# Kernel tuning notes

Hardware: AMD Instinct MI355X
Metric: run time of the kernel (lower is better)

Reference implementation:

```python
import jax, jax.numpy as jnp
import numpy as np

EPS_KERNEL = 1e-4   # eps added inside softmax_kernel exp
EPS_DENOM = 1e-6    # eps added to k_cumsum in the denominator
N_CHUNKS = 128      # matches torch.chunk(128, dim=-2) in causal_linear_attention_noncuda


def gaussian_orthogonal_random_matrix(nb_rows, nb_cols, rng):
    # scaling=0: rows are orthogonal blocks scaled by chi-distributed norms
    n_full = nb_rows // nb_cols + (1 if nb_rows % nb_cols else 0)
    blocks = []
    for _ in range(n_full):
        g = rng.standard_normal((nb_cols, nb_cols))
        qmat, _ = np.linalg.qr(g)
        blocks.append(qmat.T)
    mat = np.concatenate(blocks, axis=0)[:nb_rows]
    multiplier = np.linalg.norm(rng.standard_normal((nb_rows, nb_cols)), axis=1)
    return (multiplier[:, None] * mat).astype(np.float32)


def softmax_kernel(x, proj, is_query):
    # x: [b,h,n,d], proj: [m,d] -> phi(x): [b,h,n,m]
    d = x.shape[-1]
    normalizer = d ** -0.25
    ratio = proj.shape[0] ** -0.5
    xd = jnp.einsum('bhnd,md->bhnm', normalizer * x, proj)
    diag = 0.5 * (normalizer ** 2) * jnp.sum(x * x, axis=-1, keepdims=True)  # [b,h,n,1]
    if is_query:
        mx = jnp.max(xd, axis=-1, keepdims=True)
    else:
        mx = jnp.max(xd, axis=(-1, -2), keepdims=True)
    return ratio * (jnp.exp(xd - diag - mx) + EPS_KERNEL)


def causal_linear_attention(q, k, v):
    # q,k: [b,h,n,m] phi-features; v: [b,h,n,d]
    b, h, n, m = q.shape
    d = v.shape[-1]
    c = n // N_CHUNKS  # chunk length

    def chunked(t):
        return jnp.moveaxis(t.reshape(b, h, N_CHUNKS, c, t.shape[-1]), 2, 0)

    qc, kc, vc = chunked(q), chunked(k), chunked(v)  # [nc,b,h,c,*]

    def step(carry, inp):
        k_last, ctx_last = carry  # [b,h,m], [b,h,m,d]
        qi, ki, vi = inp
        k_cum = k_last[:, :, None, :] + jnp.cumsum(ki, axis=2)            # [b,h,c,m]
        d_inv = 1.0 / jnp.einsum('bhcm,bhcm->bhc', qi, k_cum + EPS_DENOM)
        ctx = jnp.einsum('bhcm,bhcd->bhcmd', ki, vi)                      # [b,h,c,m,d]
        ctx_cum = ctx_last[:, :, None, :, :] + jnp.cumsum(ctx, axis=2)
        out = jnp.einsum('bhcmd,bhcm,bhc->bhcd', ctx_cum, qi, d_inv)
        return (k_cum[:, :, -1], ctx_cum[:, :, -1]), out

    init = (jnp.zeros((b, h, m), q.dtype), jnp.zeros((b, h, m, d), q.dtype))
    _, outs = jax.lax.scan(jax.checkpoint(step), init, (qc, kc, vc))
    return jnp.moveaxis(outs, 0, 2).reshape(b, h, n, d)


def setup_inputs() -> dict:
    key = jax.random.key(0)
    kq, kk, kv = jax.random.split(key, 3)
    shape = (2, 8, 2048, 64)  # [batch, heads, seq, dim_heads]
    q = jax.random.normal(kq, shape, dtype=jnp.float32)
    k = jax.random.normal(kk, shape, dtype=jnp.float32)
    v = jax.random.normal(kv, shape, dtype=jnp.float32)
    proj = jnp.asarray(gaussian_orthogonal_random_matrix(256, 64, np.random.default_rng(0)))
    return {"q": q, "k": k, "v": v, "projection_matrix": proj}


def reference(q, k, v, projection_matrix):
    q_prime = softmax_kernel(q, projection_matrix, is_query=True)
    k_prime = softmax_kernel(k, projection_matrix, is_query=False)
    return causal_linear_attention(q_prime, k_prime, v)
```

## Files before the change

### kernel.cpp

```cpp
#include <hip/hip_runtime.h>
#include <hip/hip_bf16.h>
#include <cstddef>

typedef __attribute__((ext_vector_type(8))) short bf16x8;
typedef __attribute__((ext_vector_type(4))) float f32x4;

#define NCH_ 512
#define NRM_ 0.35355339059327373f
#define RATIO_ 0.0625f
#define EPSC_ 6.25e-6f
#define MFMA(a,b,c) __builtin_amdgcn_mfma_f32_16x16x32_bf16((a),(b),(c),0,0,0)

__device__ __forceinline__ unsigned short f2b(float f) {
  unsigned u = __float_as_uint(f);
  u += 0x7FFFu + ((u >> 16) & 1u);
  return (unsigned short)(u >> 16);
}
__device__ __forceinline__ float b2f(unsigned short h) {
  return __uint_as_float(((unsigned)h) << 16);
}
__device__ __forceinline__ unsigned pk2f(float a, float b) {
  union { __hip_bfloat162 h; unsigned u; } cv;
  cv.h = __float22bfloat162_rn(make_float2(a, b));
  return cv.u;
}
__device__ __forceinline__ float sumsq4(float4 a){ return a.x*a.x+a.y*a.y+a.z*a.z+a.w*a.w; }

__device__ __forceinline__ void gbar(unsigned* cnt, unsigned goal) {
  __syncthreads();
  if (threadIdx.x == 0) {
    __threadfence();
    __hip_atomic_fetch_add(cnt, 1u, __ATOMIC_RELEASE, __HIP_MEMORY_SCOPE_AGENT);
    while (__hip_atomic_fetch_add(cnt, 0u, __ATOMIC_RELAXED, __HIP_MEMORY_SCOPE_AGENT) < goal)
      __builtin_amdgcn_s_sleep(2);
    __threadfence();
  }
  __syncthreads();
}

__global__ __launch_bounds__(256, 2) void fused_kernel(
    const float* __restrict__ qg, const float* __restrict__ kg,
    const float* __restrict__ vg, const float* __restrict__ projg,
    unsigned short* __restrict__ kvxP, unsigned short* __restrict__ sxP,
    float* __restrict__ blockmax, float* __restrict__ vsumG,
    float* __restrict__ out_g, unsigned* __restrict__ barcnt)
{
  __shared__ unsigned short R0[256*72];
  __shared__ unsigned short XB[128*72];
  __shared__ unsigned short C_[80*72];
  __shared__ float diagK[64];
  __shared__ float diagQ[64];
  __shared__ float rmS[4*64];
  __shared__ float cmS[4];
  __shared__ float schS;
  const int t=threadIdx.x, ch=blockIdx.x;
  const int row0 = ch*64;
  const int lane=t&63, m16=lane&15, q4=lane>>4, w=t>>6;
  const int f0 = w*64, r0 = w*16;
  unsigned short* KX = XB;
  unsigned short* QX = XB + 64*72;
  unsigned short* kpT = XB;

#pragma unroll
  for (int i=0;i<8;++i){ int flat=i*2048+t*8; int f=flat>>6, d2=flat&63;
    float4 p0 = *(const float4*)(projg+flat);
    float4 p1 = *(const float4*)(projg+flat+4);
    *(uint4*)&R0[f*72+d2] = make_uint4(pk2f(p0.x,p0.y),pk2f(p0.z,p0.w),
                                       pk2f(p1.x,p1.y),pk2f(p1.z,p1.w)); }
  {
    const float* xg = kg + (size_t)row0*64;
#pragma unroll
    for (int i=0;i<4;++i){
      int flat=i*1024+t*4; int r=flat>>6, d2=flat&63;
      float4 f = *(const float4*)(xg+flat);
      float ss = sumsq4(f);
      ss += __shfl_xor(ss,1); ss += __shfl_xor(ss,2);
      ss += __shfl_xor(ss,4); ss += __shfl_xor(ss,8);
      if ((t&15)==0) diagK[r] = 0.0625f*ss;
      *(uint2*)&KX[r*72+d2] = make_uint2(pk2f(NRM_*f.x,NRM_*f.y), pk2f(NRM_*f.z,NRM_*f.w));
    }
  }
  {
    const float* xg = qg + (size_t)row0*64;
#pragma unroll
    for (int i=0;i<4;++i){
      int flat=i*1024+t*4; int r=flat>>6, d2=flat&63;
      float4 f = *(const float4*)(xg+flat);
      float ss = sumsq4(f);
      ss += __shfl_xor(ss,1); ss += __shfl_xor(ss,2);
      ss += __shfl_xor(ss,4); ss += __shfl_xor(ss,8);
      if ((t&15)==0) diagQ[r] = 0.0625f*ss;
      *(uint2*)&QX[r*72+d2] = make_uint2(pk2f(NRM_*f.x,NRM_*f.y), pk2f(NRM_*f.z,NRM_*f.w));
    }
  }
  {
    int c = t&63, sq_ = t>>6;
#pragma unroll
    for (int i=0;i<16;++i)
      C_[c*72 + sq_*16 + i] = f2b(vg[((size_t)row0 + sq_*16 + i)*64 + c]);
    int cc = 64 + (t>>4), s4 = (t&15)*4;
    unsigned short hv = (cc==64) ? (unsigned short)0x3F80 : (unsigned short)0;
    unsigned pv = (unsigned)hv | ((unsigned)hv<<16);
    *(uint2*)&C_[cc*72 + s4] = make_uint2(pv, pv);
  }
  __syncthreads();

  if (t < 80) {
    float s = 0.f;
#pragma unroll 16
    for (int i=0;i<64;++i) s += b2f(C_[t*72+i]);
    vsumG[(size_t)ch*80 + t] = s;
  }

  bf16x8 bk[4][2], bq[4][2]; float dk4[4], dq4[4];
#pragma unroll
  for (int rt=0;rt<4;++rt){
    bk[rt][0] = *(const bf16x8*)&KX[(rt*16+m16)*72 + q4*8];
    bk[rt][1] = *(const bf16x8*)&KX[(rt*16+m16)*72 + 32 + q4*8];
    bq[rt][0] = *(const bf16x8*)&QX[(rt*16+m16)*72 + q4*8];
    bq[rt][1] = *(const bf16x8*)&QX[(rt*16+m16)*72 + 32 + q4*8];
    dk4[rt] = diagK[rt*16+m16];
    dq4[rt] = diagQ[rt*16+m16];
  }
  f32x4 kacc[4][4], qacc[4][4];
#pragma unroll
  for (int rt=0;rt<4;++rt)
#pragma unroll
    for (int mt=0;mt<4;++mt){ kacc[rt][mt] = (f32x4){0.f,0.f,0.f,0.f};
                              qacc[rt][mt] = (f32x4){0.f,0.f,0.f,0.f}; }
#pragma unroll
  for (int kk=0;kk<2;++kk)
#pragma unroll
    for (int mt=0;mt<4;++mt){
      bf16x8 a = *(const bf16x8*)&R0[(f0+mt*16+m16)*72 + kk*32 + q4*8];
#pragma unroll
      for (int rt=0;rt<4;++rt){
        kacc[rt][mt] = MFMA(a, bk[rt][kk], kacc[rt][mt]);
        qacc[rt][mt] = MFMA(a, bq[rt][kk], qacc[rt][mt]);
      }
    }
  {
    float mx = kacc[0][0][0];
#pragma unroll
    for (int rt=0;rt<4;++rt)
#pragma unroll
      for (int mt=0;mt<4;++mt)
#pragma unroll
        for (int j=0;j<4;++j) mx = fmaxf(mx, kacc[rt][mt][j]);
#pragma unroll
    for (int off=1; off<64; off<<=1) mx = fmaxf(mx, __shfl_xor(mx, off));
    if (lane == 0) cmS[w] = mx;
  }
#pragma unroll
  for (int rt=0;rt<4;++rt){
    float p = qacc[rt][0][0];
#pragma unroll
    for (int mt=0;mt<4;++mt)
#pragma unroll
      for (int j=0;j<4;++j) p = fmaxf(p, qacc[rt][mt][j]);
    p = fmaxf(p, __shfl_xor(p,16)); p = fmaxf(p, __shfl_xor(p,32));
    if (q4 == 0) rmS[w*64 + rt*16+m16] = p;
  }
  __syncthreads();
  const float cmax = fmaxf(fmaxf(cmS[0],cmS[1]),fmaxf(cmS[2],cmS[3]));
  if (t == 0) blockmax[ch] = cmax;

  unsigned short* qS = R0;
#pragma unroll
  for (int rt=0;rt<4;++rt){
    int rr = rt*16+m16;
    float rm = fmaxf(fmaxf(rmS[rr],rmS[64+rr]),fmaxf(rmS[128+rr],rmS[192+rr]));
    float e = dq4[rt] + rm;
#pragma unroll
    for (int mt=0;mt<4;++mt){
      float v0 = RATIO_*(__expf(qacc[rt][mt][0]-e)+1e-4f);
      float v1 = RATIO_*(__expf(qacc[rt][mt][1]-e)+1e-4f);
      float v2 = RATIO_*(__expf(qacc[rt][mt][2]-e)+1e-4f);
      float v3 = RATIO_*(__expf(qacc[rt][mt][3]-e)+1e-4f);
      *(uint2*)&qS[rr*264 + f0 + mt*16 + q4*4] = make_uint2(pk2f(v0,v1), pk2f(v2,v3));
    }
  }
  __syncthreads();
  bf16x8 aq[8];
#pragma unroll
  for (int kk=0;kk<8;++kk)
    aq[kk] = *(const bf16x8*)&qS[(r0+m16)*264 + kk*32 + q4*8];
  float q1v = 0.f;
#pragma unroll
  for (int kk=0;kk<8;++kk){
    union { bf16x8 v; unsigned u[4]; } av; av.v = aq[kk];
#pragma unroll
    for (int i=0;i<4;++i)
      q1v += b2f((unsigned short)av.u[i]) + b2f((unsigned short)(av.u[i]>>16));
  }
  q1v += __shfl_xor(q1v,16); q1v += __shfl_xor(q1v,32);
  __syncthreads();

  unsigned short* kpS = R0;
  unsigned kpx[4][4][2];
#pragma unroll
  for (int rt=0;rt<4;++rt){
    float e = dk4[rt] + cmax;
    int rr = rt*16+m16;
#pragma unroll
    for (int mt=0;mt<4;++mt){
      float v0 = RATIO_*__expf(kacc[rt][mt][0]-e);
      float v1 = RATIO_*__expf(kacc[rt][mt][1]-e);
      float v2 = RATIO_*__expf(kacc[rt][mt][2]-e);
      float v3 = RATIO_*__expf(kacc[rt][mt][3]-e);
      kpx[rt][mt][0] = pk2f(v0,v1); kpx[rt][mt][1] = pk2f(v2,v3);
      *(uint2*)&kpS[rr*264 + f0 + mt*16 + q4*4] = make_uint2(kpx[rt][mt][0], kpx[rt][mt][1]);
    }
  }
  if ((w>>1) == 0) {
#pragma unroll
    for (int rt=0;rt<4;++rt)
#pragma unroll
      for (int mt=0;mt<4;++mt)
#pragma unroll
        for (int jp=0;jp<2;++jp){
          int frl = (w&1)*64 + mt*16 + q4*4 + jp*2;
          unsigned uv = kpx[rt][mt][jp];
          kpT[frl*72 + rt*16+m16]     = (unsigned short)uv;
          kpT[(frl+1)*72 + rt*16+m16] = (unsigned short)(uv>>16);
        }
  }
  __syncthreads();
#pragma unroll
  for (int h=0; h<2; ++h) {
    if (h == 1) {
      __syncthreads();
      if ((w>>1) == 1) {
#pragma unroll
        for (int rt=0;rt<4;++rt)
#pragma unroll
          for (int mt=0;mt<4;++mt)
#pragma unroll
            for (int jp=0;jp<2;++jp){
              int frl = (w&1)*64 + mt*16 + q4*4 + jp*2;
              unsigned uv = kpx[rt][mt][jp];
              kpT[frl*72 + rt*16+m16]     = (unsigned short)uv;
              kpT[(frl+1)*72 + rt*16+m16] = (unsigned short)(uv>>16);
            }
      }
      __syncthreads();
    }
    f32x4 c2a[5][2];
#pragma unroll
    for (int ct=0;ct<5;++ct)
#pragma unroll
      for (int p=0;p<2;++p) c2a[ct][p] = (f32x4){0.f,0.f,0.f,0.f};
#pragma unroll
    for (int kk=0;kk<2;++kk){
      bf16x8 av[5];
#pragma unroll
      for (int ct=0;ct<5;++ct)
        av[ct] = *(const bf16x8*)&C_[(ct*16+m16)*72 + kk*32 + q4*8];
#pragma unroll
      for (int p=0;p<2;++p){
        int mtl = w*2 + p;
        bf16x8 bv = *(const bf16x8*)&kpT[(mtl*16+m16)*72 + kk*32 + q4*8];
#pragma unroll
        for (int ct=0;ct<5;++ct)
          c2a[ct][p] = MFMA(av[ct], bv, c2a[ct][p]);
      }
    }
#pragma unroll
    for (int ct=0;ct<5;++ct)
#pragma unroll
      for (int p=0;p<2;++p){
        int mtg = h*8 + w*2 + p;
        int mrow = mtg*16 + m16;
        int fb = (mrow>>5)*512 + ((mrow>>3)&3)*8 + (mrow&7);
        unsigned short* dst = kvxP + (size_t)(ch*5+ct)*4096 + fb + (q4*4)*32;
#pragma unroll
        for (int j=0;j<4;++j)
          dst[j*32] = f2b(c2a[ct][p][j]);
      }
    if (h == 0) __syncthreads();
  }

  gbar(barcnt, (unsigned)gridDim.x);

  if (t < 32) {
    float bm = blockmax[(ch>>5)*32 + t];
    float km = bm;
#pragma unroll
    for (int off=16; off>=1; off>>=1) km = fmaxf(km, __shfl_xor(km, off));
    if (t == (ch & 31)) schS = __expf(bm - km);
  }
  if (ch < 320) {
    float* sS  = (float*)XB;
    float* vsS = ((float*)XB) + 32;
    const int qtr = ch & 3, ct5 = (ch>>2)%5, bh = ch/20;
    if (t < 32) {
      float bm = blockmax[bh*32 + t];
      float km = bm;
#pragma unroll
      for (int off=16; off>=1; off>>=1) km = fmaxf(km, __shfl_xor(km, off));
      sS[t] = __expf(bm - km);
    }
    for (int i=t; i<512; i+=256){
      int chl = i>>4, c16 = i&15;
      vsS[chl*16+c16] = vsumG[(size_t)(bh*32+chl)*80 + ct5*16 + c16];
    }
    __syncthreads();
    const int fbase = qtr*1024 + t*4;
    const int c16t = (t>>3)&15;
    const bool isEps = (ct5==4) && (c16t == 1);
    float carry0=0.f, carry1=0.f, carry2=0.f, carry3=0.f;
    const size_t stride = (size_t)5*4096;
    size_t base = ((size_t)(bh*32)*5 + ct5)*4096 + fbase;
#pragma unroll 4
    for (int chl=0; chl<32; ++chl){
      unsigned s0, s1;
      if (isEps) { unsigned ee = pk2f(1e-6f,1e-6f); s0 = ee; s1 = ee; }
      else { s0 = pk2f(carry0,carry1); s1 = pk2f(carry2,carry3); }
      *(uint2*)(sxP + base) = make_uint2(s0, s1);
      uint2 raw = *(const uint2*)(kvxP + base);
      float sc_ = sS[chl];
      float evs = EPSC_ * vsS[chl*16+c16t];
      carry0 += sc_*b2f((unsigned short)(raw.x))     + evs;
      carry1 += sc_*b2f((unsigned short)(raw.x>>16)) + evs;
      carry2 += sc_*b2f((unsigned short)(raw.y))     + evs;
      carry3 += sc_*b2f((unsigned short)(raw.y>>16)) + evs;
      base += stride;
    }
  }

  gbar(barcnt, 2u*(unsigned)gridDim.x);

  f32x4 accA[4], accO[5];
#pragma unroll
  for (int i=0;i<4;++i) accA[i] = (f32x4){0.f,0.f,0.f,0.f};
#pragma unroll
  for (int i=0;i<5;++i) accO[i] = (f32x4){0.f,0.f,0.f,0.f};
  const unsigned short* sxb = sxP + (size_t)ch*5*4096 + m16*32 + q4*8;
#pragma unroll
  for (int kk=0;kk<8;++kk){
    bf16x8 a = aq[kk];
#pragma unroll
    for (int st=0;st<4;++st){
      bf16x8 bfr = *(const bf16x8*)&kpS[(st*16+m16)*264 + kk*32 + q4*8];
      accA[st] = MFMA(a, bfr, accA[st]);
    }
#pragma unroll
    for (int ct=0;ct<5;++ct)
      accO[ct] = MFMA(a, *(const bf16x8*)(sxb + (size_t)ct*4096 + kk*512), accO[ct]);
  }
  __syncthreads();
  const float sch = schS;
  unsigned short* P = XB;
#pragma unroll
  for (int j=0;j<4;++j){
    int rr = r0 + q4*4 + j;
    float q1r = __shfl(q1v, q4*4 + j);
    float addc = EPSC_ * q1r;
#pragma unroll
    for (int st=0;st<4;++st){
      int cc = st*16 + m16;
      P[rr*72 + cc] = f2b((cc<=rr) ? (sch*accA[st][j] + addc) : 0.f);
    }
  }
#pragma unroll
  for (int k2=0;k2<2;++k2){
    bf16x8 aP = *(const bf16x8*)&P[(r0+m16)*72 + k2*32 + q4*8];
#pragma unroll
    for (int ct=0;ct<5;++ct){
      bf16x8 bfr = *(const bf16x8*)&C_[(ct*16+m16)*72 + k2*32 + q4*8];
      accO[ct] = MFMA(aP, bfr, accO[ct]);
    }
  }
  __syncthreads();
  float* oT = (float*)R0;
#pragma unroll
  for (int j=0;j<4;++j){
    float d64 = __shfl(accO[4][j], (lane & 48));
    float d65 = __shfl(accO[4][j], (lane & 48) | 1);
    float dinv = 1.f/(d64+d65);
    int rr = r0 + q4*4 + j;
#pragma unroll
    for (int ct=0;ct<4;++ct)
      oT[rr*68 + ct*16 + m16] = accO[ct][j]*dinv;
  }
  __syncthreads();
#pragma unroll
  for (int i=0;i<4;++i){ int flat=i*1024+t*4; int r=flat>>6, c2=flat&63;
    *(float4*)(out_g + (size_t)row0*64 + flat) = *(const float4*)&oT[r*68+c2]; }
}


__global__ __launch_bounds__(256, 2) void kfeat_kernel(
    const float* __restrict__ kg, const float* __restrict__ vg,
    const float* __restrict__ projg,
    unsigned short* __restrict__ kvxP,
    float* __restrict__ blockmax, float* __restrict__ vsumG)
{
  __shared__ unsigned short R0[256*72];
  __shared__ unsigned short XB[128*72];
  __shared__ unsigned short C_[80*72];
  __shared__ float diagS[64];
  __shared__ float rmS[4];
  const int t=threadIdx.x, ch=blockIdx.x;
  const int row0 = ch*64;
  const int lane=t&63, m16=lane&15, q4=lane>>4, w=t>>6;
  const int f0 = w*64;
  unsigned short* kpS = R0;
  unsigned short* xbS = XB;
  unsigned short* kpT = XB;

#pragma unroll
  for (int i=0;i<8;++i){ int flat=i*2048+t*8; int f=flat>>6, d2=flat&63;
    float4 p0 = *(const float4*)(projg+flat);
    float4 p1 = *(const float4*)(projg+flat+4);
    *(uint4*)&R0[f*72+d2] = make_uint4(pk2f(p0.x,p0.y),pk2f(p0.z,p0.w),
                                       pk2f(p1.x,p1.y),pk2f(p1.z,p1.w)); }
  {
    const float* xg = kg + (size_t)row0*64;
#pragma unroll
    for (int i=0;i<4;++i){
      int flat=i*1024+t*4; int r=flat>>6, d2=flat&63;
      float4 f = *(const float4*)(xg+flat);
      float ss = sumsq4(f);
      ss += __shfl_xor(ss,1); ss += __shfl_xor(ss,2);
      ss += __shfl_xor(ss,4); ss += __shfl_xor(ss,8);
      if ((t&15)==0) diagS[r] = 0.0625f*ss;
      *(uint2*)&xbS[r*72+d2] = make_uint2(pk2f(NRM_*f.x,NRM_*f.y), pk2f(NRM_*f.z,NRM_*f.w));
    }
  }
  {
    int c = t&63, sq_ = t>>6;
#pragma unroll
    for (int i=0;i<16;++i)
      C_[c*72 + sq_*16 + i] = f2b(vg[((size_t)row0 + sq_*16 + i)*64 + c]);
    int cc = 64 + (t>>4), s4 = (t&15)*4;
    unsigned short hv = (cc==64) ? (unsigned short)0x3F80 : (unsigned short)0;
    unsigned pv = (unsigned)hv | ((unsigned)hv<<16);
    *(uint2*)&C_[cc*72 + s4] = make_uint2(pv, pv);
  }
  __syncthreads();

  if (t < 80) {
    float s = 0.f;
#pragma unroll 16
    for (int i=0;i<64;++i) s += b2f(C_[t*72+i]);
    vsumG[(size_t)ch*80 + t] = s;
  }

  bf16x8 b[4][2]; float diag4[4];
#pragma unroll
  for (int rt=0;rt<4;++rt){
    b[rt][0] = *(const bf16x8*)&xbS[(rt*16+m16)*72 + q4*8];
    b[rt][1] = *(const bf16x8*)&xbS[(rt*16+m16)*72 + 32 + q4*8];
    diag4[rt] = diagS[rt*16+m16];
  }
  f32x4 acc[4][4];
#pragma unroll
  for (int rt=0;rt<4;++rt)
#pragma unroll
    for (int mt=0;mt<4;++mt) acc[rt][mt] = (f32x4){0.f,0.f,0.f,0.f};
#pragma unroll
  for (int kk=0;kk<2;++kk)
#pragma unroll
    for (int mt=0;mt<4;++mt){
      bf16x8 a = *(const bf16x8*)&R0[(f0+mt*16+m16)*72 + kk*32 + q4*8];
#pragma unroll
      for (int rt=0;rt<4;++rt)
        acc[rt][mt] = MFMA(a, b[rt][kk], acc[rt][mt]);
    }
  {
    float mx = acc[0][0][0];
#pragma unroll
    for (int rt=0;rt<4;++rt)
#pragma unroll
      for (int mt=0;mt<4;++mt)
#pragma unroll
        for (int j=0;j<4;++j) mx = fmaxf(mx, acc[rt][mt][j]);
#pragma unroll
    for (int off=1; off<64; off<<=1) mx = fmaxf(mx, __shfl_xor(mx, off));
    if (lane == 0) rmS[w] = mx;
  }
  __syncthreads();
  const float cmax = fmaxf(fmaxf(rmS[0],rmS[1]),fmaxf(rmS[2],rmS[3]));
  if (t == 0) blockmax[ch] = cmax;

  unsigned kpx[4][4][2];
#pragma unroll
  for (int rt=0;rt<4;++rt){
    float e = diag4[rt] + cmax;
    int rr = rt*16+m16;
#pragma unroll
    for (int mt=0;mt<4;++mt){
      float v0 = RATIO_*__expf(acc[rt][mt][0]-e);
      float v1 = RATIO_*__expf(acc[rt][mt][1]-e);
      float v2 = RATIO_*__expf(acc[rt][mt][2]-e);
      float v3 = RATIO_*__expf(acc[rt][mt][3]-e);
      kpx[rt][mt][0] = pk2f(v0,v1); kpx[rt][mt][1] = pk2f(v2,v3);
      *(uint2*)&kpS[rr*264 + f0 + mt*16 + q4*4] = make_uint2(kpx[rt][mt][0], kpx[rt][mt][1]);
    }
  }
  if ((w>>1) == 0) {
#pragma unroll
    for (int rt=0;rt<4;++rt)
#pragma unroll
      for (int mt=0;mt<4;++mt)
#pragma unroll
        for (int jp=0;jp<2;++jp){
          int frl = (w&1)*64 + mt*16 + q4*4 + jp*2;
          unsigned uv = kpx[rt][mt][jp];
          kpT[frl*72 + rt*16+m16]     = (unsigned short)uv;
          kpT[(frl+1)*72 + rt*16+m16] = (unsigned short)(uv>>16);
        }
  }
  __syncthreads();
#pragma unroll
  for (int h=0; h<2; ++h) {
    if (h == 1) {
      __syncthreads();
      if ((w>>1) == 1) {
#pragma unroll
        for (int rt=0;rt<4;++rt)
#pragma unroll
          for (int mt=0;mt<4;++mt)
#pragma unroll
            for (int jp=0;jp<2;++jp){
              int frl = (w&1)*64 + mt*16 + q4*4 + jp*2;
              unsigned uv = kpx[rt][mt][jp];
              kpT[frl*72 + rt*16+m16]     = (unsigned short)uv;
              kpT[(frl+1)*72 + rt*16+m16] = (unsigned short)(uv>>16);
            }
      }
      __syncthreads();
    }
    f32x4 c2a[5][2];
#pragma unroll
    for (int ct=0;ct<5;++ct)
#pragma unroll
      for (int p=0;p<2;++p) c2a[ct][p] = (f32x4){0.f,0.f,0.f,0.f};
#pragma unroll
    for (int kk=0;kk<2;++kk){
      bf16x8 av[5];
#pragma unroll
      for (int ct=0;ct<5;++ct)
        av[ct] = *(const bf16x8*)&C_[(ct*16+m16)*72 + kk*32 + q4*8];
#pragma unroll
      for (int p=0;p<2;++p){
        int mtl = w*2 + p;
        bf16x8 bv = *(const bf16x8*)&kpT[(mtl*16+m16)*72 + kk*32 + q4*8];
#pragma unroll
        for (int ct=0;ct<5;++ct)
          c2a[ct][p] = MFMA(av[ct], bv, c2a[ct][p]);
      }
    }
#pragma unroll
    for (int ct=0;ct<5;++ct)
#pragma unroll
      for (int p=0;p<2;++p){
        int mtg = h*8 + w*2 + p;
        int mrow = mtg*16 + m16;
        int fb = (mrow>>5)*512 + ((mrow>>3)&3)*8 + (mrow&7);
        unsigned short* dst = kvxP + (size_t)(ch*5+ct)*4096 + fb + (q4*4)*32;
#pragma unroll
        for (int j=0;j<4;++j)
          dst[j*32] = f2b(c2a[ct][p][j]);
      }
    if (h == 0) __syncthreads();
  }
}

__global__ __launch_bounds__(256, 4) void scan_kernel(
    const unsigned short* __restrict__ kvxP, unsigned short* __restrict__ sxP,
    const float* __restrict__ blockmax, const float* __restrict__ vsumG)
{
  __shared__ float sS[32];
  __shared__ float vsS[32][16];
  const int t = threadIdx.x, bid = blockIdx.x;
  const int qtr = bid & 3, ct = (bid>>2)%5, bh = bid/20;
  if (t < 32) {
    float bm = blockmax[bh*32 + t];
    float km = bm;
#pragma unroll
    for (int off=16; off>=1; off>>=1) km = fmaxf(km, __shfl_xor(km, off));
    sS[t] = __expf(bm - km);
  }
  for (int i=t; i<512; i+=256){
    int chl = i>>4, c16 = i&15;
    vsS[chl][c16] = vsumG[(size_t)(bh*32+chl)*80 + ct*16 + c16];
  }
  __syncthreads();
  const int fbase = qtr*1024 + t*4;
  const int c16t = (t>>3)&15;
  const bool isEps = (ct==4) && (c16t == 1);
  float carry0=0.f, carry1=0.f, carry2=0.f, carry3=0.f;
  const size_t stride = (size_t)5*4096;
  size_t base = ((size_t)(bh*32)*5 + ct)*4096 + fbase;
#pragma unroll 4
  for (int chl=0; chl<32; ++chl){
    unsigned s0, s1;
    if (isEps) { unsigned ee = pk2f(1e-6f,1e-6f); s0 = ee; s1 = ee; }
    else { s0 = pk2f(carry0,carry1); s1 = pk2f(carry2,carry3); }
    *(uint2*)(sxP + base) = make_uint2(s0, s1);
    uint2 raw = *(const uint2*)(kvxP + base);
    float sch = sS[chl];
    float evs = EPSC_ * vsS[chl][c16t];
    carry0 += sch*b2f((unsigned short)(raw.x))     + evs;
    carry1 += sch*b2f((unsigned short)(raw.x>>16)) + evs;
    carry2 += sch*b2f((unsigned short)(raw.y))     + evs;
    carry3 += sch*b2f((unsigned short)(raw.y>>16)) + evs;
    base += stride;
  }
}

__global__ __launch_bounds__(256, 2) void out_kernel(
    const float* __restrict__ qg, const float* __restrict__ kg,
    const float* __restrict__ projg, const unsigned short* __restrict__ sxP,
    const float* __restrict__ vg, const float* __restrict__ blockmax,
    float* __restrict__ out_g)
{
  __shared__ unsigned short R0[256*72];
  __shared__ unsigned short KX[64*72];
  __shared__ unsigned short QX[64*72];
  __shared__ unsigned short C_[80*72];
  __shared__ float diagK[64];
  __shared__ float diagQ[64];
  __shared__ float rmS[4*64];
  __shared__ float cmS[4];
  __shared__ float schS;
  const int t=threadIdx.x, ch=blockIdx.x;
  const int row0 = ch*64;
  const int lane=t&63, m16=lane&15, q4=lane>>4, w=t>>6;
  const int f0 = w*64, r0 = w*16;
  unsigned short* P = KX;

#pragma unroll
  for (int i=0;i<8;++i){ int flat=i*2048+t*8; int f=flat>>6, d2=flat&63;
    float4 p0 = *(const float4*)(projg+flat);
    float4 p1 = *(const float4*)(projg+flat+4);
    *(uint4*)&R0[f*72+d2] = make_uint4(pk2f(p0.x,p0.y),pk2f(p0.z,p0.w),
                                       pk2f(p1.x,p1.y),pk2f(p1.z,p1.w)); }
  {
    const float* xg = kg + (size_t)row0*64;
#pragma unroll
    for (int i=0;i<4;++i){
      int flat=i*1024+t*4; int r=flat>>6, d2=flat&63;
      float4 f = *(const float4*)(xg+flat);
      float ss = sumsq4(f);
      ss += __shfl_xor(ss,1); ss += __shfl_xor(ss,2);
      ss += __shfl_xor(ss,4); ss += __shfl_xor(ss,8);
      if ((t&15)==0) diagK[r] = 0.0625f*ss;
      *(uint2*)&KX[r*72+d2] = make_uint2(pk2f(NRM_*f.x,NRM_*f.y), pk2f(NRM_*f.z,NRM_*f.w));
    }
  }
  {
    const float* xg = qg + (size_t)row0*64;
#pragma unroll
    for (int i=0;i<4;++i){
      int flat=i*1024+t*4; int r=flat>>6, d2=flat&63;
      float4 f = *(const float4*)(xg+flat);
      float ss = sumsq4(f);
      ss += __shfl_xor(ss,1); ss += __shfl_xor(ss,2);
      ss += __shfl_xor(ss,4); ss += __shfl_xor(ss,8);
      if ((t&15)==0) diagQ[r] = 0.0625f*ss;
      *(uint2*)&QX[r*72+d2] = make_uint2(pk2f(NRM_*f.x,NRM_*f.y), pk2f(NRM_*f.z,NRM_*f.w));
    }
  }
  {
    int c = t&63, sq_ = t>>6;
#pragma unroll
    for (int i=0;i<16;++i)
      C_[c*72 + sq_*16 + i] = f2b(vg[((size_t)row0 + sq_*16 + i)*64 + c]);
    int cc = 64 + (t>>4), s4 = (t&15)*4;
    unsigned short hv = (cc==64) ? (unsigned short)0x3F80 : (unsigned short)0;
    unsigned pv = (unsigned)hv | ((unsigned)hv<<16);
    *(uint2*)&C_[cc*72 + s4] = make_uint2(pv, pv);
  }
  if (t < 32) {
    float bm = blockmax[(ch>>5)*32 + t];
    float km = bm;
#pragma unroll
    for (int off=16; off>=1; off>>=1) km = fmaxf(km, __shfl_xor(km, off));
    if (t == (ch & 31)) schS = __expf(bm - km);
  }
  __syncthreads();

  bf16x8 bk[4][2], bq[4][2]; float dk4[4], dq4[4];
#pragma unroll
  for (int rt=0;rt<4;++rt){
    bk[rt][0] = *(const bf16x8*)&KX[(rt*16+m16)*72 + q4*8];
    bk[rt][1] = *(const bf16x8*)&KX[(rt*16+m16)*72 + 32 + q4*8];
    bq[rt][0] = *(const bf16x8*)&QX[(rt*16+m16)*72 + q4*8];
    bq[rt][1] = *(const bf16x8*)&QX[(rt*16+m16)*72 + 32 + q4*8];
    dk4[rt] = diagK[rt*16+m16];
    dq4[rt] = diagQ[rt*16+m16];
  }
  f32x4 kacc[4][4], qacc[4][4];
#pragma unroll
  for (int rt=0;rt<4;++rt)
#pragma unroll
    for (int mt=0;mt<4;++mt){ kacc[rt][mt] = (f32x4){0.f,0.f,0.f,0.f};
                              qacc[rt][mt] = (f32x4){0.f,0.f,0.f,0.f}; }
#pragma unroll
  for (int kk=0;kk<2;++kk)
#pragma unroll
    for (int mt=0;mt<4;++mt){
      bf16x8 a = *(const bf16x8*)&R0[(f0+mt*16+m16)*72 + kk*32 + q4*8];
#pragma unroll
      for (int rt=0;rt<4;++rt){
        kacc[rt][mt] = MFMA(a, bk[rt][kk], kacc[rt][mt]);
        qacc[rt][mt] = MFMA(a, bq[rt][kk], qacc[rt][mt]);
      }
    }
  {
    float mx = kacc[0][0][0];
#pragma unroll
    for (int rt=0;rt<4;++rt)
#pragma unroll
      for (int mt=0;mt<4;++mt)
#pragma unroll
        for (int j=0;j<4;++j) mx = fmaxf(mx, kacc[rt][mt][j]);
#pragma unroll
    for (int off=1; off<64; off<<=1) mx = fmaxf(mx, __shfl_xor(mx, off));
    if (lane == 0) cmS[w] = mx;
  }
#pragma unroll
  for (int rt=0;rt<4;++rt){
    float p = qacc[rt][0][0];
#pragma unroll
    for (int mt=0;mt<4;++mt)
#pragma unroll
      for (int j=0;j<4;++j) p = fmaxf(p, qacc[rt][mt][j]);
    p = fmaxf(p, __shfl_xor(p,16)); p = fmaxf(p, __shfl_xor(p,32));
    if (q4 == 0) rmS[w*64 + rt*16+m16] = p;
  }
  __syncthreads();
  const float cmax = fmaxf(fmaxf(cmS[0],cmS[1]),fmaxf(cmS[2],cmS[3]));

  unsigned short* qS = R0;
#pragma unroll
  for (int rt=0;rt<4;++rt){
    int rr = rt*16+m16;
    float rm = fmaxf(fmaxf(rmS[rr],rmS[64+rr]),fmaxf(rmS[128+rr],rmS[192+rr]));
    float e = dq4[rt] + rm;
#pragma unroll
    for (int mt=0;mt<4;++mt){
      float v0 = RATIO_*(__expf(qacc[rt][mt][0]-e)+1e-4f);
      float v1 = RATIO_*(__expf(qacc[rt][mt][1]-e)+1e-4f);
      float v2 = RATIO_*(__expf(qacc[rt][mt][2]-e)+1e-4f);
      float v3 = RATIO_*(__expf(qacc[rt][mt][3]-e)+1e-4f);
      *(uint2*)&qS[rr*264 + f0 + mt*16 + q4*4] = make_uint2(pk2f(v0,v1), pk2f(v2,v3));
    }
  }
  __syncthreads();
  bf16x8 aq[8];
#pragma unroll
  for (int kk=0;kk<8;++kk)
    aq[kk] = *(const bf16x8*)&qS[(r0+m16)*264 + kk*32 + q4*8];
  float q1v = 0.f;
#pragma unroll
  for (int kk=0;kk<8;++kk){
    union { bf16x8 v; unsigned u[4]; } av; av.v = aq[kk];
#pragma unroll
    for (int i=0;i<4;++i)
      q1v += b2f((unsigned short)av.u[i]) + b2f((unsigned short)(av.u[i]>>16));
  }
  q1v += __shfl_xor(q1v,16); q1v += __shfl_xor(q1v,32);
  __syncthreads();

  unsigned short* kpS = R0;
#pragma unroll
  for (int rt=0;rt<4;++rt){
    float e = dk4[rt] + cmax;
    int rr = rt*16+m16;
#pragma unroll
    for (int mt=0;mt<4;++mt){
      float v0 = RATIO_*__expf(kacc[rt][mt][0]-e);
      float v1 = RATIO_*__expf(kacc[rt][mt][1]-e);
      float v2 = RATIO_*__expf(kacc[rt][mt][2]-e);
      float v3 = RATIO_*__expf(kacc[rt][mt][3]-e);
      *(uint2*)&kpS[rr*264 + f0 + mt*16 + q4*4] = make_uint2(pk2f(v0,v1), pk2f(v2,v3));
    }
  }
  __syncthreads();

  f32x4 accA[4], accO[5];
#pragma unroll
  for (int i=0;i<4;++i) accA[i] = (f32x4){0.f,0.f,0.f,0.f};
#pragma unroll
  for (int i=0;i<5;++i) accO[i] = (f32x4){0.f,0.f,0.f,0.f};
  const unsigned short* sxb = sxP + (size_t)ch*5*4096 + m16*32 + q4*8;
#pragma unroll
  for (int kk=0;kk<8;++kk){
    bf16x8 a = aq[kk];
#pragma unroll
    for (int st=0;st<4;++st){
      bf16x8 bfr = *(const bf16x8*)&kpS[(st*16+m16)*264 + kk*32 + q4*8];
      accA[st] = MFMA(a, bfr, accA[st]);
    }
#pragma unroll
    for (int ct=0;ct<5;++ct)
      accO[ct] = MFMA(a, *(const bf16x8*)(sxb + (size_t)ct*4096 + kk*512), accO[ct]);
  }
  __syncthreads();
  const float sch = schS;
#pragma unroll
  for (int j=0;j<4;++j){
    int rr = r0 + q4*4 + j;
    float q1r = __shfl(q1v, q4*4 + j);
    float addc = EPSC_ * q1r;
#pragma unroll
    for (int st=0;st<4;++st){
      int cc = st*16 + m16;
      P[rr*72 + cc] = f2b((cc<=rr) ? (sch*accA[st][j] + addc) : 0.f);
    }
  }
#pragma unroll
  for (int k2=0;k2<2;++k2){
    bf16x8 aP = *(const bf16x8*)&P[(r0+m16)*72 + k2*32 + q4*8];
#pragma unroll
    for (int ct=0;ct<5;++ct){
      bf16x8 bfr = *(const bf16x8*)&C_[(ct*16+m16)*72 + k2*32 + q4*8];
      accO[ct] = MFMA(aP, bfr, accO[ct]);
    }
  }
  __syncthreads();
  float* oT = (float*)R0;
#pragma unroll
  for (int j=0;j<4;++j){
    float d64 = __shfl(accO[4][j], (lane & 48));
    float d65 = __shfl(accO[4][j], (lane & 48) | 1);
    float dinv = 1.f/(d64+d65);
    int rr = r0 + q4*4 + j;
#pragma unroll
    for (int ct=0;ct<4;++ct)
      oT[rr*68 + ct*16 + m16] = accO[ct][j]*dinv;
  }
  __syncthreads();
#pragma unroll
  for (int i=0;i<4;++i){ int flat=i*1024+t*4; int r=flat>>6, c2=flat&63;
    *(float4*)(out_g + (size_t)row0*64 + flat) = *(const float4*)&oT[r*68+c2]; }
}

extern "C" void kernel_launch(void* const* d_in, const int* in_sizes, int n_in,
                              void* d_out, int out_size, void* d_ws, size_t ws_size,
                              hipStream_t stream)
{
  (void)in_sizes; (void)n_in; (void)out_size; (void)ws_size;
  const float* q    = (const float*)d_in[0];
  const float* k    = (const float*)d_in[1];
  const float* v    = (const float*)d_in[2];
  const float* proj = (const float*)d_in[3];
  float* out = (float*)d_out;

  char* p8 = (char*)d_ws;
  unsigned short* kvxP = (unsigned short*)p8; p8 += (size_t)NCH_*5*4096*2;
  unsigned short* sxP  = (unsigned short*)p8; p8 += (size_t)NCH_*5*4096*2;
  float* blockmax = (float*)p8; p8 += NCH_*sizeof(float);
  float* vsumG    = (float*)p8; p8 += (size_t)NCH_*80*sizeof(float);
  unsigned* barcnt = (unsigned*)p8;

  static int fused_ok = -1;
  if (fused_ok < 0) {
    int nb = 0;
    hipError_t e = hipOccupancyMaxActiveBlocksPerMultiprocessor(&nb, fused_kernel,
                                                                256, (size_t)0);
    fused_ok = (e == hipSuccess && nb >= 2) ? 1 : 0;
  }

  if (fused_ok) {
    hipMemsetAsync(barcnt, 0, sizeof(unsigned), stream);
    fused_kernel<<<dim3(NCH_), dim3(256), 0, stream>>>(q, k, v, proj, kvxP, sxP,
                                                       blockmax, vsumG, out, barcnt);
  } else {
    kfeat_kernel<<<dim3(NCH_), dim3(256), 0, stream>>>(k, v, proj, kvxP,
                                                       blockmax, vsumG);
    scan_kernel <<<dim3(320),  dim3(256), 0, stream>>>(kvxP, sxP, blockmax, vsumG);
    out_kernel  <<<dim3(NCH_), dim3(256), 0, stream>>>(q, k, proj, sxP, v,
                                                       blockmax, out);
  }
}
```

Baseline: 115.2 us.

## Replace grid-wide barriers with per-(batch,head) arrival counters in fused kernel

The two global grid barriers become per-(batch,head) counters. Scan blocks wait only for the 32 feature blocks of their own head, and output blocks wait only for the 20 scan blocks that cover their head. This lets heads proceed independently and removes whole-grid stalls, at the cost of 32 counters to reset and more complex dependency logic. The scan loop unroll also rises from 4 to 8, and the spin-wait uses an atomic load with a longer sleep.

```diff
diff --git a/kernel.cpp b/kernel.cpp
--- a/kernel.cpp
+++ b/kernel.cpp
@@ -26,13 +26,17 @@
 }
 __device__ __forceinline__ float sumsq4(float4 a){ return a.x*a.x+a.y*a.y+a.z*a.z+a.w*a.w; }
 
-__device__ __forceinline__ void gbar(unsigned* cnt, unsigned goal) {
+__device__ __forceinline__ void arrive(unsigned* cnt) {
   __syncthreads();
   if (threadIdx.x == 0) {
     __threadfence();
     __hip_atomic_fetch_add(cnt, 1u, __ATOMIC_RELEASE, __HIP_MEMORY_SCOPE_AGENT);
-    while (__hip_atomic_fetch_add(cnt, 0u, __ATOMIC_RELAXED, __HIP_MEMORY_SCOPE_AGENT) < goal)
-      __builtin_amdgcn_s_sleep(2);
+  }
+}
+__device__ __forceinline__ void wait_for(unsigned* cnt, unsigned goal) {
+  if (threadIdx.x == 0) {
+    while (__hip_atomic_load(cnt, __ATOMIC_RELAXED, __HIP_MEMORY_SCOPE_AGENT) < goal)
+      __builtin_amdgcn_s_sleep(4);
     __threadfence();
   }
   __syncthreads();
@@ -43,7 +47,7 @@
     const float* __restrict__ vg, const float* __restrict__ projg,
     unsigned short* __restrict__ kvxP, unsigned short* __restrict__ sxP,
     float* __restrict__ blockmax, float* __restrict__ vsumG,
-    float* __restrict__ out_g, unsigned* __restrict__ barcnt)
+    float* __restrict__ out_g, unsigned* __restrict__ cnts)
 {
   __shared__ unsigned short R0[256*72];
   __shared__ unsigned short XB[128*72];
@@ -57,6 +61,9 @@
   const int row0 = ch*64;
   const int lane=t&63, m16=lane&15, q4=lane>>4, w=t>>6;
   const int f0 = w*64, r0 = w*16;
+  const int bh_own = ch>>5;
+  unsigned* cntA = cnts;
+  unsigned* cntS = cnts + 16;
   unsigned short* KX = XB;
   unsigned short* QX = XB + 64*72;
   unsigned short* kpT = XB;
@@ -280,21 +287,15 @@
     if (h == 0) __syncthreads();
   }
 
-  gbar(barcnt, (unsigned)gridDim.x);
-
-  if (t < 32) {
-    float bm = blockmax[(ch>>5)*32 + t];
-    float km = bm;
-#pragma unroll
-    for (int off=16; off>=1; off>>=1) km = fmaxf(km, __shfl_xor(km, off));
-    if (t == (ch & 31)) schS = __expf(bm - km);
-  }
+  arrive(&cntA[bh_own]);
+
   if (ch < 320) {
+    const int qtr = ch & 3, ct5 = (ch>>2)%5, bhs = ch/20;
+    wait_for(&cntA[bhs], 32u);
     float* sS  = (float*)XB;
     float* vsS = ((float*)XB) + 32;
-    const int qtr = ch & 3, ct5 = (ch>>2)%5, bh = ch/20;
     if (t < 32) {
-      float bm = blockmax[bh*32 + t];
+      float bm = blockmax[bhs*32 + t];
       float km = bm;
 #pragma unroll
       for (int off=16; off>=1; off>>=1) km = fmaxf(km, __shfl_xor(km, off));
@@ -302,7 +303,7 @@
     }
     for (int i=t; i<512; i+=256){
       int chl = i>>4, c16 = i&15;
-      vsS[chl*16+c16] = vsumG[(size_t)(bh*32+chl)*80 + ct5*16 + c16];
+      vsS[chl*16+c16] = vsumG[(size_t)(bhs*32+chl)*80 + ct5*16 + c16];
     }
     __syncthreads();
     const int fbase = qtr*1024 + t*4;
@@ -310,8 +311,8 @@
     const bool isEps = (ct5==4) && (c16t == 1);
     float carry0=0.f, carry1=0.f, carry2=0.f, carry3=0.f;
     const size_t stride = (size_t)5*4096;
-    size_t base = ((size_t)(bh*32)*5 + ct5)*4096 + fbase;
-#pragma unroll 4
+    size_t base = ((size_t)(bhs*32)*5 + ct5)*4096 + fbase;
+#pragma unroll 8
     for (int chl=0; chl<32; ++chl){
       unsigned s0, s1;
       if (isEps) { unsigned ee = pk2f(1e-6f,1e-6f); s0 = ee; s1 = ee; }
@@ -326,9 +327,18 @@
       carry3 += sc_*b2f((unsigned short)(raw.y>>16)) + evs;
       base += stride;
     }
-  }
-
-  gbar(barcnt, 2u*(unsigned)gridDim.x);
+    arrive(&cntS[bhs]);
+  }
+
+  wait_for(&cntS[bh_own], 20u);
+
+  if (t < 32) {
+    float bm = blockmax[bh_own*32 + t];
+    float km = bm;
+#pragma unroll
+    for (int off=16; off>=1; off>>=1) km = fmaxf(km, __shfl_xor(km, off));
+    if (t == (ch & 31)) schS = __expf(bm - km);
+  }
 
   f32x4 accA[4], accO[5];
 #pragma unroll
@@ -856,7 +866,7 @@
   unsigned short* sxP  = (unsigned short*)p8; p8 += (size_t)NCH_*5*4096*2;
   float* blockmax = (float*)p8; p8 += NCH_*sizeof(float);
   float* vsumG    = (float*)p8; p8 += (size_t)NCH_*80*sizeof(float);
-  unsigned* barcnt = (unsigned*)p8;
+  unsigned* cnts  = (unsigned*)p8;
 
   static int fused_ok = -1;
   if (fused_ok < 0) {
@@ -867,9 +877,9 @@
   }
 
   if (fused_ok) {
-    hipMemsetAsync(barcnt, 0, sizeof(unsigned), stream);
+    hipMemsetAsync(cnts, 0, 32*sizeof(unsigned), stream);
     fused_kernel<<<dim3(NCH_), dim3(256), 0, stream>>>(q, k, v, proj, kvxP, sxP,
-                                                       blockmax, vsumG, out, barcnt);
+                                                       blockmax, vsumG, out, cnts);
   } else {
     kfeat_kernel<<<dim3(NCH_), dim3(256), 0, stream>>>(k, v, proj, kvxP,
                                                        blockmax, vsumG);
```

Result: no change. 115.2 us (+0.0%).
